# Kernel optimization log

Hardware: AMD Instinct MI355X
Metric: run time of the kernel (lower is better)

Reference implementation:

```python
import jax, jax.numpy as jnp
import numpy as np

N_NODES = 50000
N_EDGES = 1600000
N_DECODE = 500000
D = 128
EPS = 1e-6


def _sage_conv(x, src, dst, Wl, bl, Wr, n_nodes):
    # PyG SAGEConv (mean aggr): out = lin_l(mean_{j in N(i)} x_j) + lin_r(x_i)
    msg = x[src]                                            # [E, D] gather
    s = jax.ops.segment_sum(msg, dst, num_segments=n_nodes) # [N, D]
    cnt = jax.ops.segment_sum(jnp.ones((src.shape[0],), x.dtype), dst,
                              num_segments=n_nodes)         # [N]
    aggr = s / jnp.maximum(cnt, 1.0)[:, None]
    return aggr @ Wl + bl + x @ Wr


def setup_inputs() -> dict:
    key = jax.random.key(0)
    ks = jax.random.split(key, 9)
    scale = 1.0 / np.sqrt(D)
    x = jax.random.normal(ks[0], (N_NODES, D), dtype=jnp.float32)
    edge_index = jax.random.randint(ks[1], (2, N_EDGES), 0, N_NODES, dtype=jnp.int64)
    decode_index = jax.random.randint(ks[2], (2, N_DECODE), 0, N_NODES, dtype=jnp.int64)
    W1l = jax.random.normal(ks[3], (D, D), dtype=jnp.float32) * scale
    b1 = jnp.zeros((D,), dtype=jnp.float32)
    W1r = jax.random.normal(ks[4], (D, D), dtype=jnp.float32) * scale
    W2l = jax.random.normal(ks[5], (D, D), dtype=jnp.float32) * scale
    b2 = jnp.zeros((D,), dtype=jnp.float32)
    W2r = jax.random.normal(ks[6], (D, D), dtype=jnp.float32) * scale
    return {"x": x, "edge_index": edge_index, "decode_index": decode_index,
            "W1l": W1l, "b1": b1, "W1r": W1r, "W2l": W2l, "b2": b2, "W2r": W2r}


def reference(x, edge_index, decode_index, W1l, b1, W1r, W2l, b2, W2r):
    src, dst = edge_index[0], edge_index[1]
    h = _sage_conv(x, src, dst, W1l, b1, W1r, N_NODES)
    h = jax.nn.relu(h)
    # dropout is a no-op in eval mode (training=False)
    h = _sage_conv(h, src, dst, W2l, b2, W2r, N_NODES)
    a = h[decode_index[0]]                                  # [Dk, D]
    b = h[decode_index[1]]
    num = jnp.sum(a * b, axis=1)
    denom = jnp.maximum(jnp.linalg.norm(a, axis=1) * jnp.linalg.norm(b, axis=1), EPS)
    return jax.nn.sigmoid(num / denom)
```

## Files before the change

kernel.cpp:

```cpp
#include <hip/hip_runtime.h>
#include <hip/hip_bf16.h>
#include <cstddef>

#define D 128
#define NBITS 8
#define BCAP 12288
#define CHUNK 4096
#define TSHIFT 14

typedef float floatx4 __attribute__((ext_vector_type(4)));
typedef float floatx2 __attribute__((ext_vector_type(2)));

__device__ __forceinline__ int incl_scan64(int v) {
    const int lane = threadIdx.x & 63;
#pragma unroll
    for (int o = 1; o < 64; o <<= 1) {
        int u = __shfl_up(v, o);
        if (lane >= o) v += u;
    }
    return v;
}

__global__ void prep_kernel(const float* __restrict__ x, unsigned* __restrict__ xf8,
                            int nq, int nblk_a, int nblk_b,
                            const float* __restrict__ W1l, const float* __restrict__ W1r,
                            const float* __restrict__ W2l, const float* __restrict__ W2r,
                            unsigned* __restrict__ Wtf8, int* __restrict__ zero_base,
                            int nzero) {
    int blk = (int)blockIdx.x;
    if (blk < nblk_a) {
        int t = blk * 256 + threadIdx.x;
        if (t < nq) {
            float4 v = ((const float4*)x)[t];
            int lo = __builtin_amdgcn_cvt_pk_fp8_f32(v.x, v.y, 0, false);
            xf8[t] = (unsigned)__builtin_amdgcn_cvt_pk_fp8_f32(v.z, v.w, lo, true);
        }
    } else if (blk < nblk_a + nblk_b) {
        int t2 = (blk - nblk_a) * 256 + threadIdx.x;
        int widx = t2 >> 12;
        int within = t2 & 4095;
        int n = within >> 5;
        int g = within & 31;
        const float* W = (widx == 0) ? W1l : (widx == 1) ? W1r : (widx == 2) ? W2l : W2r;
        float w0 = W[(size_t)(4 * g + 0) * D + n];
        float w1 = W[(size_t)(4 * g + 1) * D + n];
        float w2 = W[(size_t)(4 * g + 2) * D + n];
        float w3 = W[(size_t)(4 * g + 3) * D + n];
        int lo = __builtin_amdgcn_cvt_pk_fp8_f32(w0, w1, 0, false);
        Wtf8[(size_t)widx * 4096 + (size_t)n * 32 + g] =
            (unsigned)__builtin_amdgcn_cvt_pk_fp8_f32(w2, w3, lo, true);
    } else {
        int t3 = (blk - nblk_a - nblk_b) * 256 + threadIdx.x;
        if (t3 < nzero) zero_base[t3] = 0;
    }
}

__global__ void __launch_bounds__(512) bucketA_kernel(
        const int* __restrict__ src, const int* __restrict__ dst,
        int* __restrict__ bucket_cursor, unsigned* __restrict__ regions,
        int n_edges, int n_buckets) {
    __shared__ int cnt[256];
    __shared__ int off[256];
    __shared__ int gbase[256];
    __shared__ int cur[256];
    __shared__ int tmp[256];
    __shared__ int bsum[4];
    __shared__ unsigned ent[CHUNK];
    __shared__ unsigned char bid[CHUNK];
    const int tid = threadIdx.x;
    const int e0 = blockIdx.x * CHUNK;
    const int n = min(CHUNK, n_edges - e0);

    if (tid < 256) cnt[tid] = 0;
    __syncthreads();
    for (int i = tid; i < n; i += 512) {
        atomicAdd(&cnt[dst[e0 + i] >> NBITS], 1);
    }
    __syncthreads();
    if (tid < 256) {
        int v = cnt[tid];
        int s = incl_scan64(v);
        if ((tid & 63) == 63) bsum[tid >> 6] = s;
        tmp[tid] = s;
    }
    __syncthreads();
    if (tid < 256) {
        int wv = tid >> 6;
        int add = (wv > 0 ? bsum[0] : 0) + (wv > 1 ? bsum[1] : 0) + (wv > 2 ? bsum[2] : 0);
        int excl = tmp[tid] + add - cnt[tid];
        if (tid < n_buckets && cnt[tid] > 0) gbase[tid] = atomicAdd(&bucket_cursor[tid], cnt[tid]);
        else gbase[tid] = 0;
        cur[tid] = off[tid] = excl;
    }
    __syncthreads();
    for (int i = tid; i < n; i += 512) {
        int d = dst[e0 + i];
        int s = src[e0 + i];
        int b = d >> NBITS;
        int p = atomicAdd(&cur[b], 1);
        ent[p] = ((unsigned)(d & ((1 << NBITS) - 1)) << 16) | (unsigned)s;
        bid[p] = (unsigned char)b;
    }
    __syncthreads();
    for (int i = tid; i < n; i += 512) {
        int b = bid[i];
        int t = gbase[b] + (i - off[b]);
        if (t < BCAP) regions[(size_t)b * BCAP + t] = ent[i];
    }
}

__global__ void __launch_bounds__(1024) bucketB_kernel(
        const unsigned* __restrict__ regions, const int* __restrict__ bucket_cursor,
        int* __restrict__ offs4, int* __restrict__ csr_src,
        int n_buckets, int n_nodes) {
    __shared__ int ndeg[1024];
    __shared__ int ncur[1024];
    __shared__ int tmp[256];
    __shared__ int wsum[16];
    __shared__ int bsum[4];
    __shared__ int s_cbase;
    const int b = blockIdx.x;
    const int tid = threadIdx.x;
    const int count = min(bucket_cursor[b], BCAP);
    const int node0 = b << NBITS;
    const unsigned* reg = regions + (size_t)b * BCAP;

    if (tid < 256) {
        int v = (tid < n_buckets) ? min(bucket_cursor[tid], BCAP) : 0;
        int s = incl_scan64(v);
        if ((tid & 63) == 63) bsum[tid >> 6] = s;
        tmp[tid] = s;
    }
    ndeg[tid] = 0;
    __syncthreads();
    if (tid < 256) {
        int wv = tid >> 6;
        int add = (wv > 0 ? bsum[0] : 0) + (wv > 1 ? bsum[1] : 0) + (wv > 2 ? bsum[2] : 0);
        tmp[tid] += add;
    }
    __syncthreads();
    if (tid == 0) {
        s_cbase = b ? tmp[b - 1] : 0;
        if (b == 0) offs4[(size_t)4 * n_nodes] = tmp[255];
    }
    __syncthreads();

    for (int k = tid; k < count; k += 1024) {
        unsigned e = reg[k];
        int bin = (int)((e >> 16) << 2) | (int)((e & 0xffffu) >> TSHIFT);
        atomicAdd(&ndeg[bin], 1);
    }
    __syncthreads();
    {
        int v = ndeg[tid];
        int s = incl_scan64(v);
        const int wid = tid >> 6;
        if ((tid & 63) == 63) wsum[wid] = s;
        __syncthreads();
        if (tid < 16) {
            int wv = wsum[tid];
#pragma unroll
            for (int o = 1; o < 16; o <<= 1) {
                int u = __shfl_up(wv, o);
                if (tid >= o) wv += u;
            }
            wsum[tid] = wv;
        }
        __syncthreads();
        const int cbase = s_cbase;
        int excl = s + (wid ? wsum[wid - 1] : 0) - v;
        ncur[tid] = excl;
        if (node0 + (tid >> 2) < n_nodes) offs4[(node0 << 2) + tid] = cbase + excl;
    }
    __syncthreads();
    const int cbase = s_cbase;
    for (int k = tid; k < count; k += 1024) {
        unsigned e = reg[k];
        int bin = (int)((e >> 16) << 2) | (int)((e & 0xffffu) >> TSHIFT);
        int p = atomicAdd(&ncur[bin], 1);
        csr_src[cbase + p] = (int)(e & 0xffffu);
    }
}

__device__ __forceinline__ void accf8p(floatx2* a2, uint4 u) {
    unsigned w[4] = {u.x, u.y, u.z, u.w};
#pragma unroll
    for (int k = 0; k < 4; ++k) {
        a2[2 * k + 0] += __builtin_amdgcn_cvt_pk_f32_fp8((int)w[k], false);
        a2[2 * k + 1] += __builtin_amdgcn_cvt_pk_f32_fp8((int)w[k], true);
    }
}

__global__ void __launch_bounds__(256, 8) gather_kernel(
        const unsigned* __restrict__ feat8,
        const int* __restrict__ offs4,
        const int* __restrict__ csr_src,
        unsigned* __restrict__ aggf8, int n_nodes) {
    const int wid = (blockIdx.x * blockDim.x + threadIdx.x) >> 6;
    const int lane = threadIdx.x & 63;
    const int q = lane >> 3;
    const int l8 = lane & 7;
    const int node = wid * 8 + q;
    const int nc = (node < n_nodes) ? node : (n_nodes - 1);
    const unsigned* fb = feat8 + (size_t)l8 * 4;
    floatx2 a2[8];
#pragma unroll
    for (int i = 0; i < 8; ++i) a2[i] = (floatx2)(0.f);

    int4 ob = *(const int4*)(offs4 + (size_t)4 * nc);
    const int oend = offs4[(size_t)4 * nc + 4];
    const int bnd0 = ob.x, bnd1 = ob.y, bnd2 = ob.z, bnd3 = ob.w;
#pragma unroll
    for (int t = 0; t < 4; ++t) {
        int e = (t == 0) ? bnd0 : (t == 1) ? bnd1 : (t == 2) ? bnd2 : bnd3;
        const int se = (t == 0) ? bnd1 : (t == 1) ? bnd2 : (t == 2) ? bnd3 : oend;
        for (; e + 2 <= se; e += 2) {
            int s0 = csr_src[e];
            int s1 = csr_src[e + 1];
            uint4 u0 = *(const uint4*)(fb + (size_t)s0 * 32);
            uint4 u1 = *(const uint4*)(fb + (size_t)s1 * 32);
            accf8p(a2, u0);
            accf8p(a2, u1);
        }
        if (e < se) {
            int s0 = csr_src[e];
            uint4 u0 = *(const uint4*)(fb + (size_t)s0 * 32);
            accf8p(a2, u0);
        }
    }

    float r = 1.0f / fmaxf((float)(oend - bnd0), 1.0f);
    unsigned o[4];
#pragma unroll
    for (int j = 0; j < 4; ++j) {
        int lo = __builtin_amdgcn_cvt_pk_fp8_f32(a2[2 * j].x * r, a2[2 * j].y * r, 0, false);
        o[j] = (unsigned)__builtin_amdgcn_cvt_pk_fp8_f32(a2[2 * j + 1].x * r,
                                                         a2[2 * j + 1].y * r, lo, true);
    }
    if (node < n_nodes) {
        *(uint4*)(aggf8 + (size_t)node * 32 + l8 * 4) = make_uint4(o[0], o[1], o[2], o[3]);
    }
}

#define BSTRIDE8 36
__global__ void __launch_bounds__(256, 4) mfma_gemm(
        const unsigned* __restrict__ aggf8, const unsigned* __restrict__ xin8,
        const unsigned* __restrict__ Wlt, const unsigned* __restrict__ Wrt,
        const float* __restrict__ bias, unsigned char* __restrict__ outf8,
        float* __restrict__ nrm2, int n_nodes, int relu) {
    __shared__ unsigned sB[2][64 * BSTRIDE8];
    const int tid = threadIdx.x;
    const int wave = tid >> 6;
    const int lane = tid & 63;
    const int li = lane & 15;
    const int quad = lane >> 4;
    const int node0 = blockIdx.x * 64 + wave * 16;
    const int colbase = blockIdx.y * 64;

#pragma unroll
    for (int m = 0; m < 2; ++m) {
        const unsigned* Wsrc = (m ? Wrt : Wlt) + (size_t)colbase * 32;
        for (int i = tid; i < 512; i += 256) {
            int col = i >> 3;
            int c4 = (i & 7) * 4;
            uint4 v = *(const uint4*)(Wsrc + col * 32 + c4);
            *(uint4*)(&sB[m][col * BSTRIDE8 + c4]) = v;
        }
    }
    __syncthreads();

    if (node0 >= n_nodes) return;

    floatx4 acc[4];
#pragma unroll
    for (int t = 0; t < 4; ++t) acc[t] = (floatx4)(0.f);

    int arow = node0 + li;
    if (arow >= n_nodes) arow = n_nodes - 1;
    const unsigned* aptr1 = aggf8 + (size_t)arow * 32 + quad * 2;
    const unsigned* aptr2 = xin8 + (size_t)arow * 32 + quad * 2;
    const unsigned* sb0 = &sB[0][li * BSTRIDE8 + quad * 2];
    const unsigned* sb1 = &sB[1][li * BSTRIDE8 + quad * 2];

#pragma unroll
    for (int ks = 0; ks < 4; ++ks) {
        long af = *(const long*)(aptr1 + ks * 8);
#pragma unroll
        for (int ct = 0; ct < 4; ++ct) {
            long bf = *(const long*)(sb0 + ct * 16 * BSTRIDE8 + ks * 8);
            acc[ct] = __builtin_amdgcn_mfma_f32_16x16x32_fp8_fp8(af, bf, acc[ct], 0, 0, 0);
        }
    }
#pragma unroll
    for (int ks = 0; ks < 4; ++ks) {
        long af = *(const long*)(aptr2 + ks * 8);
#pragma unroll
        for (int ct = 0; ct < 4; ++ct) {
            long bf = *(const long*)(sb1 + ct * 16 * BSTRIDE8 + ks * 8);
            acc[ct] = __builtin_amdgcn_mfma_f32_16x16x32_fp8_fp8(af, bf, acc[ct], 0, 0, 0);
        }
    }

    float sq[4] = {0.f, 0.f, 0.f, 0.f};
#pragma unroll
    for (int ct = 0; ct < 4; ++ct) {
        int col = colbase + ct * 16 + li;
        float bv = bias[col];
#pragma unroll
        for (int r = 0; r < 4; ++r) {
            int node = node0 + quad * 4 + r;
            float o = acc[ct][r] + bv;
            if (relu) o = fmaxf(o, 0.f);
            int pk = __builtin_amdgcn_cvt_pk_fp8_f32(o, o, 0, false);
            if (nrm2) {
                floatx2 dq = __builtin_amdgcn_cvt_pk_f32_fp8(pk, false);
                sq[r] += dq.x * dq.x;
            }
            if (node < n_nodes) {
                outf8[(size_t)node * D + col] = (unsigned char)(pk & 0xff);
            }
        }
    }
    if (nrm2) {
#pragma unroll
        for (int r = 0; r < 4; ++r) {
            float s = sq[r];
            s += __shfl_xor(s, 1);
            s += __shfl_xor(s, 2);
            s += __shfl_xor(s, 4);
            s += __shfl_xor(s, 8);
            int node = node0 + quad * 4 + r;
            if (li == 0 && node < n_nodes) unsafeAtomicAdd(&nrm2[node], s);
        }
    }
}

__global__ void decode_kernel(const unsigned* __restrict__ h8, const float* __restrict__ nrm2,
                              const int* __restrict__ ia, const int* __restrict__ ib,
                              float* __restrict__ out, int n_pairs) {
    int t = blockIdx.x * blockDim.x + threadIdx.x;
    int p = t >> 3;
    if (p >= n_pairs) return;
    int l8 = t & 7;
    int i0 = ia[p];
    int i1 = ib[p];
    uint4 ua = *(const uint4*)(h8 + (size_t)i0 * 32 + l8 * 4);
    uint4 ub = *(const uint4*)(h8 + (size_t)i1 * 32 + l8 * 4);
    unsigned wa[4] = {ua.x, ua.y, ua.z, ua.w};
    unsigned wb[4] = {ub.x, ub.y, ub.z, ub.w};
    float dot = 0.f;
#pragma unroll
    for (int k = 0; k < 4; ++k) {
        floatx2 alo = __builtin_amdgcn_cvt_pk_f32_fp8((int)wa[k], false);
        floatx2 ahi = __builtin_amdgcn_cvt_pk_f32_fp8((int)wa[k], true);
        floatx2 blo = __builtin_amdgcn_cvt_pk_f32_fp8((int)wb[k], false);
        floatx2 bhi = __builtin_amdgcn_cvt_pk_f32_fp8((int)wb[k], true);
        dot = fmaf(alo.x, blo.x, dot);
        dot = fmaf(alo.y, blo.y, dot);
        dot = fmaf(ahi.x, bhi.x, dot);
        dot = fmaf(ahi.y, bhi.y, dot);
    }
    dot += __shfl_xor(dot, 1);
    dot += __shfl_xor(dot, 2);
    dot += __shfl_xor(dot, 4);
    if (l8 == 0) {
        float denom = fmaxf(sqrtf(nrm2[i0] * nrm2[i1]), 1e-6f);
        float s = dot / denom;
        out[p] = 1.0f / (1.0f + expf(-s));
    }
}

extern "C" void kernel_launch(void* const* d_in, const int* in_sizes, int n_in,
                              void* d_out, int out_size, void* d_ws, size_t ws_size,
                              hipStream_t stream) {
    const float* x   = (const float*)d_in[0];
    const int*   ei  = (const int*)d_in[1];
    const int*   di  = (const int*)d_in[2];
    const float* W1l = (const float*)d_in[3];
    const float* b1  = (const float*)d_in[4];
    const float* W1r = (const float*)d_in[5];
    const float* W2l = (const float*)d_in[6];
    const float* b2  = (const float*)d_in[7];
    const float* W2r = (const float*)d_in[8];

    const int N = in_sizes[0] / D;
    const int E = in_sizes[1] / 2;
    const int K = in_sizes[2] / 2;
    const size_t NQ = (size_t)N * (D / 4);
    const int NB = (N + 255) >> 8;

    const int* src  = ei;
    const int* dstp = ei + E;
    const int* dia  = di;
    const int* dib  = di + K;

    int* bucket_cursor = (int*)d_ws;
    float* nrm2        = (float*)(bucket_cursor + 256);
    int* offs4         = (int*)(nrm2 + N);
    int* csr_src       = offs4 + 4 * N + 64;
    unsigned* xf8      = (unsigned*)(csr_src + E);
    unsigned* h1f8     = xf8 + NQ;
    unsigned* h2f8     = h1f8 + NQ;
    unsigned* Wtf8     = h2f8 + NQ;
    unsigned* W1lt     = Wtf8;
    unsigned* W1rt     = Wtf8 + 4096;
    unsigned* W2lt     = Wtf8 + 8192;
    unsigned* W2rt     = Wtf8 + 12288;
    unsigned* regions  = Wtf8 + 16384;
    unsigned* aggf8    = regions;

    float* out = (float*)d_out;

    const int nq = (int)NQ;
    const int nblk_a = (nq + 255) / 256;
    const int nblk_b = 64;
    const int nzero = 256 + N;
    const int nblk_c = (nzero + 255) / 256;
    prep_kernel<<<nblk_a + nblk_b + nblk_c, 256, 0, stream>>>(
        x, xf8, nq, nblk_a, nblk_b, W1l, W1r, W2l, W2r, Wtf8, bucket_cursor, nzero);

    const int gridA = (E + CHUNK - 1) / CHUNK;
    bucketA_kernel<<<gridA, 512, 0, stream>>>(src, dstp, bucket_cursor, regions, E, NB);
    bucketB_kernel<<<NB, 1024, 0, stream>>>(regions, bucket_cursor, offs4, csr_src, NB, N);

    const int gather_waves = (N + 7) / 8;
    const int gather_blocks = (gather_waves * 64 + 255) / 256;
    const dim3 gemm_grid((N + 63) / 64, 2);

    gather_kernel<<<gather_blocks, 256, 0, stream>>>(xf8, offs4, csr_src, aggf8, N);
    mfma_gemm<<<gemm_grid, 256, 0, stream>>>(aggf8, xf8, W1lt, W1rt, b1,
                                             (unsigned char*)h1f8, nullptr, N, 1);

    gather_kernel<<<gather_blocks, 256, 0, stream>>>(h1f8, offs4, csr_src, aggf8, N);
    mfma_gemm<<<gemm_grid, 256, 0, stream>>>(aggf8, h1f8, W2lt, W2rt, b2,
                                             (unsigned char*)h2f8, nrm2, N, 0);

    {
        long long threads = (long long)K * 8;
        int blocks = (int)((threads + 255) / 256);
        decode_kernel<<<blocks, 256, 0, stream>>>(h2f8, nrm2, dia, dib, out, K);
    }
}
```

Baseline: 228.0 us.

## Split gather and decode into two feature-half passes to shrink working set

Each gather and the decode kernel now run as two launches, one per 64-byte half of the fp8 feature rows. Each pass touches only half of every row, so the random-access working set per pass is halved and may fit better in L2/MALL. The decode passes combine through a partial-dot buffer. The cost is reading the CSR indices and decode indices twice, writing and reading partial sums, and extra kernel launches. Each row fetch is also only half a 128-byte line, which may waste bandwidth.

```diff
diff --git a/kernel.cpp b/kernel.cpp
--- a/kernel.cpp
+++ b/kernel.cpp
@@ -7,6 +7,7 @@
 #define BCAP 12288
 #define CHUNK 4096
 #define TSHIFT 14
+#define BSTRIDE8 36
 
 typedef float floatx4 __attribute__((ext_vector_type(4)));
 typedef float floatx2 __attribute__((ext_vector_type(2)));
@@ -19,6 +20,33 @@
         if (lane >= o) v += u;
     }
     return v;
+}
+
+__device__ __forceinline__ void accf8p(floatx2* a2, uint4 u) {
+    unsigned w[4] = {u.x, u.y, u.z, u.w};
+#pragma unroll
+    for (int k = 0; k < 4; ++k) {
+        a2[2 * k + 0] += __builtin_amdgcn_cvt_pk_f32_fp8((int)w[k], false);
+        a2[2 * k + 1] += __builtin_amdgcn_cvt_pk_f32_fp8((int)w[k], true);
+    }
+}
+
+__device__ __forceinline__ float dotf8(uint4 ua, uint4 ub) {
+    unsigned wa[4] = {ua.x, ua.y, ua.z, ua.w};
+    unsigned wb[4] = {ub.x, ub.y, ub.z, ub.w};
+    float dot = 0.f;
+#pragma unroll
+    for (int k = 0; k < 4; ++k) {
+        floatx2 alo = __builtin_amdgcn_cvt_pk_f32_fp8((int)wa[k], false);
+        floatx2 ahi = __builtin_amdgcn_cvt_pk_f32_fp8((int)wa[k], true);
+        floatx2 blo = __builtin_amdgcn_cvt_pk_f32_fp8((int)wb[k], false);
+        floatx2 bhi = __builtin_amdgcn_cvt_pk_f32_fp8((int)wb[k], true);
+        dot = fmaf(alo.x, blo.x, dot);
+        dot = fmaf(alo.y, blo.y, dot);
+        dot = fmaf(ahi.x, bhi.x, dot);
+        dot = fmaf(ahi.y, bhi.y, dot);
+    }
+    return dot;
 }
 
 __global__ void prep_kernel(const float* __restrict__ x, unsigned* __restrict__ xf8,
@@ -182,54 +210,41 @@
     }
 }
 
-__device__ __forceinline__ void accf8p(floatx2* a2, uint4 u) {
-    unsigned w[4] = {u.x, u.y, u.z, u.w};
-#pragma unroll
-    for (int k = 0; k < 4; ++k) {
-        a2[2 * k + 0] += __builtin_amdgcn_cvt_pk_f32_fp8((int)w[k], false);
-        a2[2 * k + 1] += __builtin_amdgcn_cvt_pk_f32_fp8((int)w[k], true);
-    }
-}
-
-__global__ void __launch_bounds__(256, 8) gather_kernel(
+__global__ void __launch_bounds__(256, 8) gather_half_kernel(
         const unsigned* __restrict__ feat8,
         const int* __restrict__ offs4,
         const int* __restrict__ csr_src,
-        unsigned* __restrict__ aggf8, int n_nodes) {
+        unsigned* __restrict__ aggf8, int n_nodes, int half) {
     const int wid = (blockIdx.x * blockDim.x + threadIdx.x) >> 6;
     const int lane = threadIdx.x & 63;
-    const int q = lane >> 3;
-    const int l8 = lane & 7;
-    const int node = wid * 8 + q;
+    const int q = lane >> 2;
+    const int l4 = lane & 3;
+    const int node = wid * 16 + q;
+    if (node - q >= n_nodes) return;
     const int nc = (node < n_nodes) ? node : (n_nodes - 1);
-    const unsigned* fb = feat8 + (size_t)l8 * 4;
+    const unsigned* fb = feat8 + (size_t)half * 16 + (size_t)l4 * 4;
     floatx2 a2[8];
 #pragma unroll
     for (int i = 0; i < 8; ++i) a2[i] = (floatx2)(0.f);
 
-    int4 ob = *(const int4*)(offs4 + (size_t)4 * nc);
-    const int oend = offs4[(size_t)4 * nc + 4];
-    const int bnd0 = ob.x, bnd1 = ob.y, bnd2 = ob.z, bnd3 = ob.w;
-#pragma unroll
-    for (int t = 0; t < 4; ++t) {
-        int e = (t == 0) ? bnd0 : (t == 1) ? bnd1 : (t == 2) ? bnd2 : bnd3;
-        const int se = (t == 0) ? bnd1 : (t == 1) ? bnd2 : (t == 2) ? bnd3 : oend;
-        for (; e + 2 <= se; e += 2) {
-            int s0 = csr_src[e];
-            int s1 = csr_src[e + 1];
-            uint4 u0 = *(const uint4*)(fb + (size_t)s0 * 32);
-            uint4 u1 = *(const uint4*)(fb + (size_t)s1 * 32);
-            accf8p(a2, u0);
-            accf8p(a2, u1);
-        }
-        if (e < se) {
-            int s0 = csr_src[e];
-            uint4 u0 = *(const uint4*)(fb + (size_t)s0 * 32);
-            accf8p(a2, u0);
-        }
-    }
-
-    float r = 1.0f / fmaxf((float)(oend - bnd0), 1.0f);
+    const int beg = offs4[(size_t)4 * nc];
+    const int end = offs4[(size_t)4 * nc + 4];
+    int e = beg;
+    for (; e + 2 <= end; e += 2) {
+        int s0 = csr_src[e];
+        int s1 = csr_src[e + 1];
+        uint4 u0 = *(const uint4*)(fb + (size_t)s0 * 32);
+        uint4 u1 = *(const uint4*)(fb + (size_t)s1 * 32);
+        accf8p(a2, u0);
+        accf8p(a2, u1);
+    }
+    if (e < end) {
+        int s0 = csr_src[e];
+        uint4 u0 = *(const uint4*)(fb + (size_t)s0 * 32);
+        accf8p(a2, u0);
+    }
+
+    float r = 1.0f / fmaxf((float)(end - beg), 1.0f);
     unsigned o[4];
 #pragma unroll
     for (int j = 0; j < 4; ++j) {
@@ -238,11 +253,11 @@
                                                          a2[2 * j + 1].y * r, lo, true);
     }
     if (node < n_nodes) {
-        *(uint4*)(aggf8 + (size_t)node * 32 + l8 * 4) = make_uint4(o[0], o[1], o[2], o[3]);
-    }
-}
-
-#define BSTRIDE8 36
+        *(uint4*)(aggf8 + (size_t)node * 32 + (size_t)half * 16 + l4 * 4) =
+            make_uint4(o[0], o[1], o[2], o[3]);
+    }
+}
+
 __global__ void __launch_bounds__(256, 4) mfma_gemm(
         const unsigned* __restrict__ aggf8, const unsigned* __restrict__ xin8,
         const unsigned* __restrict__ Wlt, const unsigned* __restrict__ Wrt,
@@ -335,38 +350,32 @@
     }
 }
 
-__global__ void decode_kernel(const unsigned* __restrict__ h8, const float* __restrict__ nrm2,
-                              const int* __restrict__ ia, const int* __restrict__ ib,
-                              float* __restrict__ out, int n_pairs) {
+__global__ void decode_half_kernel(const unsigned* __restrict__ h8,
+                                   const float* __restrict__ nrm2,
+                                   const int* __restrict__ ia, const int* __restrict__ ib,
+                                   float* __restrict__ partial, float* __restrict__ out,
+                                   int n_pairs, int half) {
     int t = blockIdx.x * blockDim.x + threadIdx.x;
-    int p = t >> 3;
+    int p = t >> 2;
     if (p >= n_pairs) return;
-    int l8 = t & 7;
+    int l4 = t & 3;
     int i0 = ia[p];
     int i1 = ib[p];
-    uint4 ua = *(const uint4*)(h8 + (size_t)i0 * 32 + l8 * 4);
-    uint4 ub = *(const uint4*)(h8 + (size_t)i1 * 32 + l8 * 4);
-    unsigned wa[4] = {ua.x, ua.y, ua.z, ua.w};
-    unsigned wb[4] = {ub.x, ub.y, ub.z, ub.w};
-    float dot = 0.f;
-#pragma unroll
-    for (int k = 0; k < 4; ++k) {
-        floatx2 alo = __builtin_amdgcn_cvt_pk_f32_fp8((int)wa[k], false);
-        floatx2 ahi = __builtin_amdgcn_cvt_pk_f32_fp8((int)wa[k], true);
-        floatx2 blo = __builtin_amdgcn_cvt_pk_f32_fp8((int)wb[k], false);
-        floatx2 bhi = __builtin_amdgcn_cvt_pk_f32_fp8((int)wb[k], true);
-        dot = fmaf(alo.x, blo.x, dot);
-        dot = fmaf(alo.y, blo.y, dot);
-        dot = fmaf(ahi.x, bhi.x, dot);
-        dot = fmaf(ahi.y, bhi.y, dot);
-    }
+    const unsigned* hb = h8 + (size_t)half * 16 + (size_t)l4 * 4;
+    uint4 ua = *(const uint4*)(hb + (size_t)i0 * 32);
+    uint4 ub = *(const uint4*)(hb + (size_t)i1 * 32);
+    float dot = dotf8(ua, ub);
     dot += __shfl_xor(dot, 1);
     dot += __shfl_xor(dot, 2);
-    dot += __shfl_xor(dot, 4);
-    if (l8 == 0) {
-        float denom = fmaxf(sqrtf(nrm2[i0] * nrm2[i1]), 1e-6f);
-        float s = dot / denom;
-        out[p] = 1.0f / (1.0f + expf(-s));
+    if (l4 == 0) {
+        if (half == 0) {
+            partial[p] = dot;
+        } else {
+            dot += partial[p];
+            float denom = fmaxf(sqrtf(nrm2[i0] * nrm2[i1]), 1e-6f);
+            float s = dot / denom;
+            out[p] = 1.0f / (1.0f + expf(-s));
+        }
     }
 }
 
@@ -402,12 +411,9 @@
     unsigned* h1f8     = xf8 + NQ;
     unsigned* h2f8     = h1f8 + NQ;
     unsigned* Wtf8     = h2f8 + NQ;
-    unsigned* W1lt     = Wtf8;
-    unsigned* W1rt     = Wtf8 + 4096;
-    unsigned* W2lt     = Wtf8 + 8192;
-    unsigned* W2rt     = Wtf8 + 12288;
     unsigned* regions  = Wtf8 + 16384;
     unsigned* aggf8    = regions;
+    float* partial     = (float*)regions;
 
     float* out = (float*)d_out;
 
@@ -423,21 +429,26 @@
     bucketA_kernel<<<gridA, 512, 0, stream>>>(src, dstp, bucket_cursor, regions, E, NB);
     bucketB_kernel<<<NB, 1024, 0, stream>>>(regions, bucket_cursor, offs4, csr_src, NB, N);
 
-    const int gather_waves = (N + 7) / 8;
+    const int gather_waves = (N + 15) / 16;
     const int gather_blocks = (gather_waves * 64 + 255) / 256;
     const dim3 gemm_grid((N + 63) / 64, 2);
 
-    gather_kernel<<<gather_blocks, 256, 0, stream>>>(xf8, offs4, csr_src, aggf8, N);
-    mfma_gemm<<<gemm_grid, 256, 0, stream>>>(aggf8, xf8, W1lt, W1rt, b1,
+    gather_half_kernel<<<gather_blocks, 256, 0, stream>>>(xf8, offs4, csr_src, aggf8, N, 0);
+    gather_half_kernel<<<gather_blocks, 256, 0, stream>>>(xf8, offs4, csr_src, aggf8, N, 1);
+    mfma_gemm<<<gemm_grid, 256, 0, stream>>>(aggf8, xf8, Wtf8, Wtf8 + 4096, b1,
                                              (unsigned char*)h1f8, nullptr, N, 1);
 
-    gather_kernel<<<gather_blocks, 256, 0, stream>>>(h1f8, offs4, csr_src, aggf8, N);
-    mfma_gemm<<<gemm_grid, 256, 0, stream>>>(aggf8, h1f8, W2lt, W2rt, b2,
+    gather_half_kernel<<<gather_blocks, 256, 0, stream>>>(h1f8, offs4, csr_src, aggf8, N, 0);
+    gather_half_kernel<<<gather_blocks, 256, 0, stream>>>(h1f8, offs4, csr_src, aggf8, N, 1);
+    mfma_gemm<<<gemm_grid, 256, 0, stream>>>(aggf8, h1f8, Wtf8 + 8192, Wtf8 + 12288, b2,
                                              (unsigned char*)h2f8, nrm2, N, 0);
 
     {
-        long long threads = (long long)K * 8;
+        long long threads = (long long)K * 4;
         int blocks = (int)((threads + 255) / 256);
-        decode_kernel<<<blocks, 256, 0, stream>>>(h2f8, nrm2, dia, dib, out, K);
-    }
-}
+        decode_half_kernel<<<blocks, 256, 0, stream>>>(h2f8, nrm2, dia, dib,
+                                                       partial, out, K, 0);
+        decode_half_kernel<<<blocks, 256, 0, stream>>>(h2f8, nrm2, dia, dib,
+                                                       partial, out, K, 1);
+    }
+}
```

New measurement: 261.8 us. +14.8%, slower.
